# Kernel optimization log

Hardware: AMD Instinct MI355X
Metric: run time of the kernel (lower is better)

## Reference

```python
import jax, jax.numpy as jnp
import numpy as np

B, S, D = 2, 2048, 1024
H = 16
HD = D // H  # 64


def setup_inputs() -> dict:
    key = jax.random.key(0)
    k = jax.random.split(key, 6)
    s = 0.02
    return {
        "x": jax.random.normal(k[0], (B, S, D), dtype=jnp.float32),
        "wq": jax.random.normal(k[1], (D, D), dtype=jnp.float32) * s,
        "wk": jax.random.normal(k[2], (D, D), dtype=jnp.float32) * s,
        "wv": jax.random.normal(k[3], (D, D), dtype=jnp.float32) * s,
        "wo": jax.random.normal(k[4], (D, D), dtype=jnp.float32) * s,
        "bo": jnp.zeros((D,), dtype=jnp.float32),
    }


def reference(x, wq, wk, wv, wo, bo):
    b, n, d = x.shape
    # nn.Linear: y = x @ W.T (qkv_bias=False)
    def proj(w):
        y = jnp.einsum('bnd,od->bno', x, w)
        return y.reshape(b, n, H, HD).transpose(0, 2, 1, 3)  # (b, H, n, hd)
    q, k, v = proj(wq), proj(wk), proj(wv)
    scores = jnp.einsum('bhqd,bhkd->bhqk', q, k) / jnp.sqrt(jnp.float32(HD))
    # NOTE: source code slices the causal mask but never applies it; softmax is unmasked.
    attn = jax.nn.softmax(scores, axis=-1)
    # dropout p=0.0 -> identity
    ctx = jnp.einsum('bhqk,bhkd->bhqd', attn, v)
    ctx = ctx.transpose(0, 2, 1, 3).reshape(b, n, d)
    return jnp.einsum('bnd,od->bno', ctx, wo) + bo
```

## Files before the change

kernel.cpp:

```cpp
#include <hip/hip_runtime.h>
#include <hip/hip_bf16.h>
#include <stdint.h>

typedef __attribute__((ext_vector_type(8))) short short8;
typedef __attribute__((ext_vector_type(4))) float float4v;
typedef __attribute__((ext_vector_type(4))) unsigned short ushort4v;

#define Bq 2
#define Sq 2048
#define Dq 1024
#define Hq 16
#define HDq 64

#define QSCALE 0.18033688011112042f

__device__ __forceinline__ unsigned short f2bf(float f) {
  union { float f; uint32_t u; } v; v.f = f;
  uint32_t r = (v.u + 0x7FFFu + ((v.u >> 16) & 1u)) >> 16;
  return (unsigned short)r;
}

__device__ __forceinline__ uint32_t pk2bf(float a, float b) {
  union { __hip_bfloat162 h; uint32_t u; } cv;
  cv.h = __float22bfloat162_rn(make_float2(a, b));
  return cv.u;
}

__device__ __forceinline__ void gl_lds16(const unsigned short* g, unsigned short* l) {
  __builtin_amdgcn_global_load_lds(
      (const __attribute__((address_space(1))) void*)g,
      (__attribute__((address_space(3))) void*)l, 16, 0, 0);
}

__global__ __launch_bounds__(256) void cvt_all_kernel(
    const float* __restrict__ x,
    const float* __restrict__ w0, const float* __restrict__ w1,
    const float* __restrict__ w2, const float* __restrict__ w3,
    unsigned short* __restrict__ xb, unsigned short* __restrict__ wb) {
  const int bid = blockIdx.x;
  const float* src;
  unsigned short* dst;
  int idx;
  if (bid < 4096) {
    src = x; dst = xb;
    idx = bid * 256 + threadIdx.x;
  } else {
    int j = (bid - 4096) * 256 + threadIdx.x;
    int z = j >> 18;
    src = (z == 0) ? w0 : (z == 1) ? w1 : (z == 2) ? w2 : w3;
    dst = wb + (size_t)z * 1048576;
    idx = j & 262143;
  }
  float4v f = ((const float4v*)src)[idx];
  ushort4v o;
#pragma unroll
  for (int q = 0; q < 4; q++) o[q] = f2bf(f[q]);
  ((ushort4v*)dst)[idx] = o;
}

template <bool OUTPROJ, int MT>
__global__ __launch_bounds__(256) void gemm_bt_kernel(
    const unsigned short* __restrict__ A,
    const unsigned short* __restrict__ W0,
    const unsigned short* __restrict__ W1,
    const unsigned short* __restrict__ W2,
    unsigned short* __restrict__ q_dst,
    unsigned short* __restrict__ k_dst,
    unsigned short* __restrict__ v_dst,
    float* __restrict__ f_dst,
    const float* __restrict__ bias) {
  constexpr int K = 1024;
  constexpr int NMB = MT / 32;
  constexpr int APASS = MT / 32;
  const int z = blockIdx.z;
  const unsigned short* W = (z == 0) ? W0 : (z == 1) ? W1 : W2;
  unsigned short* qkv = (z == 0) ? q_dst : (z == 1) ? k_dst : v_dst;

  __shared__ unsigned short Asm[MT * 64];
  __shared__ unsigned short Bsm[128 * 64];

  const int t = threadIdx.x;
  const int wave = t >> 6, lane = t & 63;
  const int quad = lane >> 4, l16 = lane & 15;
  const int wy = wave >> 1, wx = wave & 1;
  const int row0 = blockIdx.x * MT;
  const int col0 = blockIdx.y * 128;

  float4v zero = {0.f, 0.f, 0.f, 0.f};
  float4v acc[NMB][4];
#pragma unroll
  for (int i = 0; i < NMB; i++)
#pragma unroll
    for (int j = 0; j < 4; j++) acc[i][j] = zero;

  const int srow = t >> 3;
  const int sgl = ((t & 7) ^ (srow & 7)) << 3;
  const unsigned short* gA[APASS];
  const unsigned short* gB[4];
#pragma unroll
  for (int i = 0; i < APASS; i++)
    gA[i] = A + (size_t)(row0 + i * 32 + srow) * K + sgl;
#pragma unroll
  for (int i = 0; i < 4; i++)
    gB[i] = W + (size_t)(col0 + i * 32 + srow) * K + sgl;

  const int swl = (l16 & 7);

  for (int k0 = 0; k0 < K; k0 += 64) {
#pragma unroll
    for (int i = 0; i < APASS; i++) gl_lds16(gA[i] + k0, &Asm[i * 2048 + t * 8]);
#pragma unroll
    for (int i = 0; i < 4; i++) gl_lds16(gB[i] + k0, &Bsm[i * 2048 + t * 8]);
    __syncthreads();
    short8 af[NMB][2], bf[4][2];
#pragma unroll
    for (int ks = 0; ks < 2; ks++) {
#pragma unroll
      for (int mb = 0; mb < NMB; mb++) {
        int row = wy * (MT / 2) + mb * 16 + l16;
        int pg = (ks * 4 + quad) ^ swl;
        af[mb][ks] = *(const short8*)(&Asm[row * 64 + pg * 8]);
      }
#pragma unroll
      for (int nb = 0; nb < 4; nb++) {
        int row = wx * 64 + nb * 16 + l16;
        int pg = (ks * 4 + quad) ^ swl;
        bf[nb][ks] = *(const short8*)(&Bsm[row * 64 + pg * 8]);
      }
    }
#pragma unroll
    for (int ks = 0; ks < 2; ks++)
#pragma unroll
      for (int mb = 0; mb < NMB; mb++)
#pragma unroll
        for (int nb = 0; nb < 4; nb++)
          acc[mb][nb] = __builtin_amdgcn_mfma_f32_16x16x32_bf16(af[mb][ks], bf[nb][ks], acc[mb][nb], 0, 0, 0);
    __syncthreads();
  }

  const float qsc = (!OUTPROJ && z == 0) ? QSCALE : 1.0f;
#pragma unroll
  for (int mb = 0; mb < NMB; mb++) {
#pragma unroll
    for (int nb = 0; nb < 4; nb++) {
#pragma unroll
      for (int r = 0; r < 4; r++) {
        int row = row0 + wy * (MT / 2) + mb * 16 + quad * 4 + r;
        int o = col0 + wx * 64 + nb * 16 + l16;
        float val = acc[mb][nb][r];
        if (OUTPROJ) {
          f_dst[(size_t)row * 1024 + o] = val + bias[o];
        } else {
          int b = row >> 11, s = row & 2047;
          int h = o >> 6, hd = o & 63;
          qkv[(size_t)((b * Hq + h) * Sq + s) * HDq + hd] = f2bf(val * qsc);
        }
      }
    }
  }
}

__global__ __launch_bounds__(512, 4) void attn_kernel(
    const unsigned short* __restrict__ Q,
    const unsigned short* __restrict__ Kg,
    const unsigned short* __restrict__ Vg,
    unsigned short* __restrict__ ctx) {
  constexpr int VSTR = 136;
  constexpr int KBUF = 8192;
  constexpr int VBUF = 8704;
  constexpr int QSTR = 132;
  __shared__ __align__(16) unsigned char smem[67584];
  unsigned short* Ksm = (unsigned short*)smem;
  unsigned short* Vsm = (unsigned short*)(smem + 32768);
  float* obuf = (float*)smem;
  float* dbuf = (float*)(smem + 33792);

  const int wgid = blockIdx.x;
  const int lid = wgid >> 3;
  const int bh = (wgid & 7) * 4 + (lid >> 4);
  const int q0 = (lid & 15) * 128;
  const int t = threadIdx.x;
  const int wave = t >> 6, lane = t & 63;
  const int quad = lane >> 4, l16 = lane & 15;
  const int wq = wave >> 1, wk = wave & 1;
  const int swl = l16 & 7;
  const int pfirst = (wave >> 1) & 1;

  const unsigned short* Qb = Q + (size_t)bh * Sq * HDq;
  const unsigned short* Kb = Kg + (size_t)bh * Sq * HDq;
  const unsigned short* Vb = Vg + (size_t)bh * Sq * HDq;

  short8 qf[2][2];
#pragma unroll
  for (int qb = 0; qb < 2; qb++)
#pragma unroll
    for (int ks = 0; ks < 2; ks++)
      qf[qb][ks] = *(const short8*)(Qb + (size_t)(q0 + wq * 32 + qb * 16 + l16) * HDq + ks * 32 + quad * 8);

  short8 ones;
#pragma unroll
  for (int j = 0; j < 8; j++) ones[j] = (short)0x3F80;

  float4v zero = {0.f, 0.f, 0.f, 0.f};
  float4v of[2][4];
  float4v dsum[2];
#pragma unroll
  for (int qb = 0; qb < 2; qb++) {
    dsum[qb] = zero;
#pragma unroll
    for (int hb = 0; hb < 4; hb++) of[qb][hb] = zero;
  }

  const int srow = t >> 3;
  const unsigned short* gK = Kb + (size_t)srow * 64 + (((t & 7) ^ (srow & 7)) << 3);

  const int vr2 = (t & 63) * 2;
  const int vc8 = (t >> 6) << 3;
  const int sig = (vr2 & ~31) + (((vr2 >> 2) & 3) << 3) + (((vr2 >> 4) & 1) << 2) + (vr2 & 3);
  const unsigned short* gV = Vb + (size_t)vr2 * HDq + vc8;

  short8 vprA0, vprA1, vprB0, vprB1;

#define VLOADA(off) do {                                             \
    const unsigned short* vp = gV + (size_t)(off) * HDq;             \
    vprA0 = *(const short8*)(vp);                                    \
    vprA1 = *(const short8*)(vp + HDq);                              \
  } while (0)

#define VLOADB(off) do {                                             \
    const unsigned short* vp = gV + (size_t)(off) * HDq;             \
    vprB0 = *(const short8*)(vp);                                    \
    vprB1 = *(const short8*)(vp + HDq);                              \
  } while (0)

#define VPACK(bufsel, r0, r1) do {                                   \
    unsigned short* vd = &Vsm[(bufsel) * VBUF + sig];                \
    _Pragma("unroll")                                                \
    for (int j = 0; j < 8; j++) {                                    \
      uint32_t pk = (uint32_t)(unsigned short)r0[j] |                \
                    ((uint32_t)(unsigned short)r1[j] << 16);         \
      *(uint32_t*)(vd + (vc8 + j) * VSTR) = pk;                      \
    }                                                                \
  } while (0)

#define KISSUE(off, bufsel) do {                                     \
    gl_lds16(gK + (size_t)(off) * 64, &Ksm[(bufsel) * KBUF + t * 8]);\
    gl_lds16(gK + (size_t)(off) * 64 + 4096,                         \
             &Ksm[(bufsel) * KBUF + 4096 + t * 8]);                  \
  } while (0)

#define PSTEP(P, BUF) do {                                                     \
    const int p_ = (P);                                                        \
    const int kb0 = (BUF) * KBUF + wk * 4096 + p_ * 2048;                      \
    short8 kf[2][2];                                                           \
    _Pragma("unroll")                                                          \
    for (int s = 0; s < 2; s++)                                                \
      _Pragma("unroll")                                                        \
      for (int ks = 0; ks < 2; ks++)                                           \
        kf[s][ks] = *(const short8*)&Ksm[kb0 + (s * 16 + l16) * 64 + ((ks * 4 + quad) ^ swl) * 8]; \
    short8 pfr[2];                                                             \
    _Pragma("unroll")                                                          \
    for (int qb = 0; qb < 2; qb++) {                                           \
      float4v sa = zero, sb = zero;                                            \
      __builtin_amdgcn_s_setprio(1);                                           \
      _Pragma("unroll")                                                        \
      for (int ks = 0; ks < 2; ks++) {                                         \
        sa = __builtin_amdgcn_mfma_f32_16x16x32_bf16(kf[0][ks], qf[qb][ks], sa, 0, 0, 0); \
        sb = __builtin_amdgcn_mfma_f32_16x16x32_bf16(kf[1][ks], qf[qb][ks], sb, 0, 0, 0); \
      }                                                                        \
      __builtin_amdgcn_s_setprio(0);                                           \
      union { uint32_t u[4]; short8 v; } pw;                                   \
      pw.u[0] = pk2bf(__builtin_amdgcn_exp2f(sa[0]), __builtin_amdgcn_exp2f(sa[1])); \
      pw.u[1] = pk2bf(__builtin_amdgcn_exp2f(sa[2]), __builtin_amdgcn_exp2f(sa[3])); \
      pw.u[2] = pk2bf(__builtin_amdgcn_exp2f(sb[0]), __builtin_amdgcn_exp2f(sb[1])); \
      pw.u[3] = pk2bf(__builtin_amdgcn_exp2f(sb[2]), __builtin_amdgcn_exp2f(sb[3])); \
      pfr[qb] = pw.v;                                                          \
    }                                                                          \
    __builtin_amdgcn_s_setprio(1);                                             \
    _Pragma("unroll")                                                          \
    for (int qb = 0; qb < 2; qb++)                                             \
      dsum[qb] = __builtin_amdgcn_mfma_f32_16x16x32_bf16(pfr[qb], ones, dsum[qb], 0, 0, 0); \
    const int vbo = (BUF) * VBUF + wk * 64 + p_ * 32 + quad * 8;               \
    _Pragma("unroll")                                                          \
    for (int hb = 0; hb < 4; hb++) {                                           \
      short8 vf = *(const short8*)&Vsm[vbo + (hb * 16 + l16) * VSTR];          \
      _Pragma("unroll")                                                        \
      for (int qb = 0; qb < 2; qb++)                                           \
        of[qb][hb] = __builtin_amdgcn_mfma_f32_16x16x32_bf16(pfr[qb], vf, of[qb][hb], 0, 0, 0); \
    }                                                                          \
    __builtin_amdgcn_s_setprio(0);                                             \
  } while (0)

  KISSUE(0, 0);
  VLOADA(0);
  VPACK(0, vprA0, vprA1);
  VLOADB(128);
  __syncthreads();
  KISSUE(128, 1);

  for (int kt = 0; kt < Sq; kt += 256) {
    if (kt + 256 < Sq) VLOADA(kt + 256);
    PSTEP(pfirst, 0);
    PSTEP(pfirst ^ 1, 0);
    if (kt + 128 < Sq) VPACK(1, vprB0, vprB1);
    __syncthreads();
    if (kt + 256 < Sq) KISSUE(kt + 256, 0);
    if (kt + 384 < Sq) VLOADB(kt + 384);
    PSTEP(pfirst, 1);
    PSTEP(pfirst ^ 1, 1);
    if (kt + 256 < Sq) VPACK(0, vprA0, vprA1);
    __syncthreads();
    if (kt + 384 < Sq) KISSUE(kt + 384, 1);
  }

  if (wk == 0) {
#pragma unroll
    for (int qb = 0; qb < 2; qb++) {
#pragma unroll
      for (int hb = 0; hb < 4; hb++)
        *(float4v*)&obuf[(hb * 16 + l16) * QSTR + wq * 32 + qb * 16 + quad * 4] = of[qb][hb];
      if (l16 == 0)
#pragma unroll
        for (int r = 0; r < 4; r++)
          dbuf[wq * 32 + qb * 16 + quad * 4 + r] = dsum[qb][r];
    }
  }
  __syncthreads();
  if (wk == 1) {
#pragma unroll
    for (int qb = 0; qb < 2; qb++) {
#pragma unroll
      for (int hb = 0; hb < 4; hb++) {
        float4v* pp = (float4v*)&obuf[(hb * 16 + l16) * QSTR + wq * 32 + qb * 16 + quad * 4];
        float4v o = *pp;
        o += of[qb][hb];
        *pp = o;
      }
      if (l16 == 0)
#pragma unroll
        for (int r = 0; r < 4; r++)
          dbuf[wq * 32 + qb * 16 + quad * 4 + r] += dsum[qb][r];
    }
  }
  __syncthreads();

  const int b = bh >> 4, h = bh & 15;
  const int qq = t & 127, hseg = t >> 7;
  const float dinv = 1.0f / dbuf[qq];
  unsigned short* cp = ctx + ((size_t)(b * Sq + q0 + qq)) * Dq + h * 64 + hseg * 16;
  short8 o8a, o8b;
#pragma unroll
  for (int j = 0; j < 8; j++) o8a[j] = (short)f2bf(obuf[(hseg * 16 + j) * QSTR + qq] * dinv);
#pragma unroll
  for (int j = 0; j < 8; j++) o8b[j] = (short)f2bf(obuf[(hseg * 16 + 8 + j) * QSTR + qq] * dinv);
  *(short8*)cp = o8a;
  *(short8*)(cp + 8) = o8b;
#undef VLOADA
#undef VLOADB
#undef VPACK
#undef KISSUE
#undef PSTEP
}

extern "C" void kernel_launch(void* const* d_in, const int* in_sizes, int n_in,
                              void* d_out, int out_size, void* d_ws, size_t ws_size,
                              hipStream_t stream) {
  (void)in_sizes; (void)n_in; (void)out_size; (void)ws_size;
  const float* x  = (const float*)d_in[0];
  const float* wq = (const float*)d_in[1];
  const float* wk = (const float*)d_in[2];
  const float* wv = (const float*)d_in[3];
  const float* wo = (const float*)d_in[4];
  const float* bo = (const float*)d_in[5];
  float* out = (float*)d_out;

  char* ws = (char*)d_ws;
  const size_t MB = 1u << 20;
  unsigned short* xb  = (unsigned short*)(ws + 0 * MB);
  unsigned short* wqb = (unsigned short*)(ws + 8 * MB);
  unsigned short* wkb = (unsigned short*)(ws + 10 * MB);
  unsigned short* wvb = (unsigned short*)(ws + 12 * MB);
  unsigned short* wob = (unsigned short*)(ws + 14 * MB);
  unsigned short* qb  = (unsigned short*)(ws + 16 * MB);
  unsigned short* kb  = (unsigned short*)(ws + 24 * MB);
  unsigned short* vb  = (unsigned short*)(ws + 32 * MB);
  unsigned short* cxb = (unsigned short*)(ws + 40 * MB);

  cvt_all_kernel<<<8192, 256, 0, stream>>>(x, wq, wk, wv, wo, xb, wqb);

  gemm_bt_kernel<false, 128><<<dim3(32, 8, 3), 256, 0, stream>>>(
      xb, wqb, wkb, wvb, qb, kb, vb, nullptr, nullptr);
  attn_kernel<<<dim3(512), 512, 0, stream>>>(qb, kb, vb, cxb);
  gemm_bt_kernel<true, 64><<<dim3(64, 8, 1), 256, 0, stream>>>(
      cxb, wob, wob, wob, nullptr, nullptr, nullptr, out, bo);
}
```

Measured before the change: 187.6 us.

## Write V pre-transposed from QKV projection and stream it via direct LDS loads

The QKV projection epilogue now writes V in a transposed, permuted [bh][hd][s] layout, so the attention kernel can load V tiles with asynchronous global-to-LDS copies like K, instead of register loads followed by manual repacking into LDS. The attention main loop becomes a single 128-key double-buffered loop, the padded V stride is dropped, and the s_setprio hints and the per-wave ordering of the two key halves are removed. This aims to cut VALU and LDS-store work and register pressure in the attention loop. In exchange the projection's V stores are strided 4-element writes, and relying on the loop barrier alone may change how well loads overlap with compute.

```diff
diff --git a/kernel.cpp b/kernel.cpp
--- a/kernel.cpp
+++ b/kernel.cpp
@@ -143,17 +143,31 @@
   for (int mb = 0; mb < NMB; mb++) {
 #pragma unroll
     for (int nb = 0; nb < 4; nb++) {
-#pragma unroll
-      for (int r = 0; r < 4; r++) {
-        int row = row0 + wy * (MT / 2) + mb * 16 + quad * 4 + r;
+      if (OUTPROJ) {
+#pragma unroll
+        for (int r = 0; r < 4; r++) {
+          int row = row0 + wy * (MT / 2) + mb * 16 + quad * 4 + r;
+          int o = col0 + wx * 64 + nb * 16 + l16;
+          f_dst[(size_t)row * 1024 + o] = acc[mb][nb][r] + bias[o];
+        }
+      } else if (z == 2) {
+        int rowb = row0 + wy * (MT / 2) + mb * 16 + quad * 4;
+        int b = rowb >> 11, s0 = rowb & 2047;
         int o = col0 + wx * 64 + nb * 16 + l16;
-        float val = acc[mb][nb][r];
-        if (OUTPROJ) {
-          f_dst[(size_t)row * 1024 + o] = val + bias[o];
-        } else {
+        int h = o >> 6, hd = o & 63;
+        int c = (s0 & ~31) + (((s0 >> 2) & 3) << 3) + (((s0 >> 4) & 1) << 2);
+        ushort4v p4;
+#pragma unroll
+        for (int r = 0; r < 4; r++) p4[r] = f2bf(acc[mb][nb][r]);
+        *(ushort4v*)(qkv + ((size_t)((b * Hq + h) * HDq + hd)) * Sq + c) = p4;
+      } else {
+#pragma unroll
+        for (int r = 0; r < 4; r++) {
+          int row = row0 + wy * (MT / 2) + mb * 16 + quad * 4 + r;
+          int o = col0 + wx * 64 + nb * 16 + l16;
           int b = row >> 11, s = row & 2047;
           int h = o >> 6, hd = o & 63;
-          qkv[(size_t)((b * Hq + h) * Sq + s) * HDq + hd] = f2bf(val * qsc);
+          qkv[(size_t)((b * Hq + h) * Sq + s) * HDq + hd] = f2bf(acc[mb][nb][r] * qsc);
         }
       }
     }
@@ -163,13 +177,12 @@
 __global__ __launch_bounds__(512, 4) void attn_kernel(
     const unsigned short* __restrict__ Q,
     const unsigned short* __restrict__ Kg,
-    const unsigned short* __restrict__ Vg,
+    const unsigned short* __restrict__ Vt,
     unsigned short* __restrict__ ctx) {
-  constexpr int VSTR = 136;
   constexpr int KBUF = 8192;
-  constexpr int VBUF = 8704;
+  constexpr int VBUF = 8192;
   constexpr int QSTR = 132;
-  __shared__ __align__(16) unsigned char smem[67584];
+  __shared__ __align__(16) unsigned char smem[65536];
   unsigned short* Ksm = (unsigned short*)smem;
   unsigned short* Vsm = (unsigned short*)(smem + 32768);
   float* obuf = (float*)smem;
@@ -184,11 +197,10 @@
   const int quad = lane >> 4, l16 = lane & 15;
   const int wq = wave >> 1, wk = wave & 1;
   const int swl = l16 & 7;
-  const int pfirst = (wave >> 1) & 1;
 
   const unsigned short* Qb = Q + (size_t)bh * Sq * HDq;
   const unsigned short* Kb = Kg + (size_t)bh * Sq * HDq;
-  const unsigned short* Vb = Vg + (size_t)bh * Sq * HDq;
+  const unsigned short* Vb = Vt + (size_t)bh * HDq * Sq;
 
   short8 qf[2][2];
 #pragma unroll
@@ -214,34 +226,8 @@
   const int srow = t >> 3;
   const unsigned short* gK = Kb + (size_t)srow * 64 + (((t & 7) ^ (srow & 7)) << 3);
 
-  const int vr2 = (t & 63) * 2;
-  const int vc8 = (t >> 6) << 3;
-  const int sig = (vr2 & ~31) + (((vr2 >> 2) & 3) << 3) + (((vr2 >> 4) & 1) << 2) + (vr2 & 3);
-  const unsigned short* gV = Vb + (size_t)vr2 * HDq + vc8;
-
-  short8 vprA0, vprA1, vprB0, vprB1;
-
-#define VLOADA(off) do {                                             \
-    const unsigned short* vp = gV + (size_t)(off) * HDq;             \
-    vprA0 = *(const short8*)(vp);                                    \
-    vprA1 = *(const short8*)(vp + HDq);                              \
-  } while (0)
-
-#define VLOADB(off) do {                                             \
-    const unsigned short* vp = gV + (size_t)(off) * HDq;             \
-    vprB0 = *(const short8*)(vp);                                    \
-    vprB1 = *(const short8*)(vp + HDq);                              \
-  } while (0)
-
-#define VPACK(bufsel, r0, r1) do {                                   \
-    unsigned short* vd = &Vsm[(bufsel) * VBUF + sig];                \
-    _Pragma("unroll")                                                \
-    for (int j = 0; j < 8; j++) {                                    \
-      uint32_t pk = (uint32_t)(unsigned short)r0[j] |                \
-                    ((uint32_t)(unsigned short)r1[j] << 16);         \
-      *(uint32_t*)(vd + (vc8 + j) * VSTR) = pk;                      \
-    }                                                                \
-  } while (0)
+  const int vrow = t >> 4;
+  const unsigned short* gV = Vb + (size_t)vrow * Sq + (((t & 15) ^ (vrow & 15)) << 3);
 
 #define KISSUE(off, bufsel) do {                                     \
     gl_lds16(gK + (size_t)(off) * 64, &Ksm[(bufsel) * KBUF + t * 8]);\
@@ -249,9 +235,14 @@
              &Ksm[(bufsel) * KBUF + 4096 + t * 8]);                  \
   } while (0)
 
+#define VISSUE(off, bufsel) do {                                     \
+    gl_lds16(gV + (off), &Vsm[(bufsel) * VBUF + t * 8]);             \
+    gl_lds16(gV + (off) + 32 * Sq,                                   \
+             &Vsm[(bufsel) * VBUF + 4096 + t * 8]);                  \
+  } while (0)
+
 #define PSTEP(P, BUF) do {                                                     \
-    const int p_ = (P);                                                        \
-    const int kb0 = (BUF) * KBUF + wk * 4096 + p_ * 2048;                      \
+    const int kb0 = (BUF) * KBUF + wk * 4096 + (P) * 2048;                     \
     short8 kf[2][2];                                                           \
     _Pragma("unroll")                                                          \
     for (int s = 0; s < 2; s++)                                                \
@@ -262,13 +253,11 @@
     _Pragma("unroll")                                                          \
     for (int qb = 0; qb < 2; qb++) {                                           \
       float4v sa = zero, sb = zero;                                            \
-      __builtin_amdgcn_s_setprio(1);                                           \
       _Pragma("unroll")                                                        \
       for (int ks = 0; ks < 2; ks++) {                                         \
         sa = __builtin_amdgcn_mfma_f32_16x16x32_bf16(kf[0][ks], qf[qb][ks], sa, 0, 0, 0); \
         sb = __builtin_amdgcn_mfma_f32_16x16x32_bf16(kf[1][ks], qf[qb][ks], sb, 0, 0, 0); \
       }                                                                        \
-      __builtin_amdgcn_s_setprio(0);                                           \
       union { uint32_t u[4]; short8 v; } pw;                                   \
       pw.u[0] = pk2bf(__builtin_amdgcn_exp2f(sa[0]), __builtin_amdgcn_exp2f(sa[1])); \
       pw.u[1] = pk2bf(__builtin_amdgcn_exp2f(sa[2]), __builtin_amdgcn_exp2f(sa[3])); \
@@ -276,41 +265,33 @@
       pw.u[3] = pk2bf(__builtin_amdgcn_exp2f(sb[2]), __builtin_amdgcn_exp2f(sb[3])); \
       pfr[qb] = pw.v;                                                          \
     }                                                                          \
-    __builtin_amdgcn_s_setprio(1);                                             \
     _Pragma("unroll")                                                          \
     for (int qb = 0; qb < 2; qb++)                                             \
       dsum[qb] = __builtin_amdgcn_mfma_f32_16x16x32_bf16(pfr[qb], ones, dsum[qb], 0, 0, 0); \
-    const int vbo = (BUF) * VBUF + wk * 64 + p_ * 32 + quad * 8;               \
     _Pragma("unroll")                                                          \
     for (int hb = 0; hb < 4; hb++) {                                           \
-      short8 vf = *(const short8*)&Vsm[vbo + (hb * 16 + l16) * VSTR];          \
+      short8 vf = *(const short8*)&Vsm[(BUF) * VBUF + (hb * 16 + l16) * 128 + ((wk * 8 + (P) * 4 + quad) ^ l16) * 8]; \
       _Pragma("unroll")                                                        \
       for (int qb = 0; qb < 2; qb++)                                           \
         of[qb][hb] = __builtin_amdgcn_mfma_f32_16x16x32_bf16(pfr[qb], vf, of[qb][hb], 0, 0, 0); \
     }                                                                          \
-    __builtin_amdgcn_s_setprio(0);                                             \
   } while (0)
 
   KISSUE(0, 0);
-  VLOADA(0);
-  VPACK(0, vprA0, vprA1);
-  VLOADB(128);
+  VISSUE(0, 0);
   __syncthreads();
   KISSUE(128, 1);
-
-  for (int kt = 0; kt < Sq; kt += 256) {
-    if (kt + 256 < Sq) VLOADA(kt + 256);
-    PSTEP(pfirst, 0);
-    PSTEP(pfirst ^ 1, 0);
-    if (kt + 128 < Sq) VPACK(1, vprB0, vprB1);
+  VISSUE(128, 1);
+
+  for (int kt = 0; kt < Sq; kt += 128) {
+    const int cur = (kt >> 7) & 1;
+    PSTEP(0, cur);
+    PSTEP(1, cur);
     __syncthreads();
-    if (kt + 256 < Sq) KISSUE(kt + 256, 0);
-    if (kt + 384 < Sq) VLOADB(kt + 384);
-    PSTEP(pfirst, 1);
-    PSTEP(pfirst ^ 1, 1);
-    if (kt + 256 < Sq) VPACK(0, vprA0, vprA1);
-    __syncthreads();
-    if (kt + 384 < Sq) KISSUE(kt + 384, 1);
+    if (kt + 256 < Sq) {
+      KISSUE(kt + 256, cur);
+      VISSUE(kt + 256, cur);
+    }
   }
 
   if (wk == 0) {
@@ -355,10 +336,8 @@
   for (int j = 0; j < 8; j++) o8b[j] = (short)f2bf(obuf[(hseg * 16 + 8 + j) * QSTR + qq] * dinv);
   *(short8*)cp = o8a;
   *(short8*)(cp + 8) = o8b;
-#undef VLOADA
-#undef VLOADB
-#undef VPACK
 #undef KISSUE
+#undef VISSUE
 #undef PSTEP
 }
 
```

Result: faster. 180.0 us (-4.0%).
